# Optimization experiments

Measured on AMD Instinct MI355X. Metric: run time of the kernel, lower is better.

The kernel has to match this reference:

```python
import jax, jax.numpy as jnp
import numpy as np

D = 2048      # d_model
QH = 32       # query heads
KVH = 8       # kv heads
HD = D // QH  # head_dim = 64
B = 2
S = 2048
THETA = 1000000.0


def _rope_cos_sin(seq_len, hd, dtype):
    inv_freq = 1.0 / (THETA ** (jnp.arange(0, hd, 2, dtype=jnp.float32) / hd))
    t = jnp.arange(seq_len, dtype=jnp.float32)
    freqs = jnp.einsum('i,j->ij', t, inv_freq)          # [S, hd/2]
    emb = jnp.concatenate([freqs, freqs], axis=-1)      # [S, hd]
    cos = jnp.cos(emb)[None, :, None, :].astype(dtype)  # [1,S,1,hd]
    sin = jnp.sin(emb)[None, :, None, :].astype(dtype)
    return cos, sin


def _rotate_half(x):
    half = x.shape[-1] // 2
    x1, x2 = x[..., :half], x[..., half:]
    return jnp.concatenate([-x2, x1], axis=-1)


def setup_inputs() -> dict:
    key = jax.random.key(0)
    ks = jax.random.split(key, 9)
    inp = {
        'q': jax.random.normal(ks[0], (B, S, D), dtype=jnp.float32),
        'k': jax.random.normal(ks[1], (B, S, D), dtype=jnp.float32),
        'v': jax.random.normal(ks[2], (B, S, D), dtype=jnp.float32),
        'attn_mask': jnp.ones((B, S), dtype=jnp.float32),  # ignored by source math
        'Wq': jax.random.normal(ks[3], (D, D), dtype=jnp.float32) * 0.02,
        'Wk': jax.random.normal(ks[4], (D, KVH * HD), dtype=jnp.float32) * 0.02,
        'Wv': jax.random.normal(ks[5], (D, KVH * HD), dtype=jnp.float32) * 0.02,
        'Wo': jax.random.normal(ks[6], (D, D), dtype=jnp.float32) * 0.02,
        'bo': jnp.zeros((D,), dtype=jnp.float32),
    }
    return inp


def reference(q, k, v, attn_mask, Wq, Wk, Wv, Wo, bo):
    b, s, _ = q.shape
    qh = (q @ Wq).reshape(b, s, QH, HD)
    kh = (k @ Wk).reshape(b, s, KVH, HD)
    vh = (v @ Wv).reshape(b, s, KVH, HD)

    cos, sin = _rope_cos_sin(s, HD, qh.dtype)
    qh = qh * cos + _rotate_half(qh) * sin
    kh = kh * cos + _rotate_half(kh) * sin

    g = QH // KVH
    # torch .repeat tiles the head axis: [h0..h7, h0..h7, ...]
    kh = jnp.tile(kh, (1, 1, g, 1))  # [b,s,QH,HD]
    vh = jnp.tile(vh, (1, 1, g, 1))

    qt = qh.transpose(0, 2, 1, 3)  # [b,QH,s,HD]
    kt = kh.transpose(0, 2, 1, 3)
    vt = vh.transpose(0, 2, 1, 3)

    scale = 1.0 / jnp.sqrt(jnp.asarray(HD, dtype=qt.dtype))
    scores = jnp.einsum('bhqd,bhkd->bhqk', qt, kt) * scale
    # source passes attn_mask=None, is_causal=False when a mask is given:
    # full non-causal attention, mask value unused.
    attn = jax.nn.softmax(scores, axis=-1)
    out = jnp.einsum('bhqk,bhkd->bhqd', attn, vt)
    out = out.transpose(0, 2, 1, 3).reshape(b, s, D)
    return out @ Wo + bo
```

## Files before the change

### kernel.cpp

```cpp
#include <hip/hip_runtime.h>
#include <math.h>

#define D_    2048
#define QH_   32
#define KVH_  8
#define HD_   64
#define B_    2
#define S_    2048
#define NROW_ (B_*S_)
#define KVD_  (KVH_*HD_)
#define LOG2E 1.44269504f

typedef __bf16 bf16;
typedef __bf16 bf16x2 __attribute__((ext_vector_type(2)));
typedef __bf16 bf16x4 __attribute__((ext_vector_type(4)));
typedef __bf16 bf16x8 __attribute__((ext_vector_type(8)));
typedef float  f32x4  __attribute__((ext_vector_type(4)));
typedef float  f32x16 __attribute__((ext_vector_type(16)));

__device__ __forceinline__ f32x4 mfma16(bf16x8 a, bf16x8 b, f32x4 c) {
  return __builtin_amdgcn_mfma_f32_16x16x32_bf16(a, b, c, 0, 0, 0);
}
__device__ __forceinline__ f32x16 mfma32(bf16x8 a, bf16x8 b, f32x16 c) {
  return __builtin_amdgcn_mfma_f32_32x32x16_bf16(a, b, c, 0, 0, 0);
}

__device__ __forceinline__ void gload_lds16(const bf16* g, bf16* l) {
  __builtin_amdgcn_global_load_lds(
      (const __attribute__((address_space(1))) void*)g,
      (__attribute__((address_space(3))) void*)l, 16, 0, 0);
}

__device__ __forceinline__ unsigned pack_bf16(float a, float b) {
  union { bf16x2 v; unsigned u; } t;
  t.v[0] = (bf16)a; t.v[1] = (bf16)b;
  return t.u;
}

__global__ void k_convert(const float* __restrict__ in, bf16* __restrict__ out, int n4) {
  int i = blockIdx.x * 256 + threadIdx.x;
  if (i >= n4) return;
  f32x4 v = ((const f32x4*)in)[i];
  bf16x4 o;
#pragma unroll
  for (int j = 0; j < 4; j++) o[j] = (bf16)v[j];
  ((bf16x4*)out)[i] = o;
}

__global__ void k_convert2(const float* __restrict__ in0, const float* __restrict__ in1,
                           bf16* __restrict__ o0, bf16* __restrict__ o1, int n4) {
  const float* in = blockIdx.z ? in1 : in0;
  bf16* out = blockIdx.z ? o1 : o0;
  int i = blockIdx.x * 256 + threadIdx.x;
  if (i >= n4) return;
  f32x4 v = ((const f32x4*)in)[i];
  bf16x4 o;
#pragma unroll
  for (int j = 0; j < 4; j++) o[j] = (bf16)v[j];
  ((bf16x4*)out)[i] = o;
}

__device__ __forceinline__ void transpose_w_body(const float* W, bf16* Wt, int K, int N) {
  __shared__ float tile[32][33];
  int n0 = blockIdx.x * 32, k0 = blockIdx.y * 32;
  int tx = threadIdx.x, ty = threadIdx.y;
#pragma unroll
  for (int j = 0; j < 4; j++)
    tile[ty + 8*j][tx] = W[(size_t)(k0 + ty + 8*j) * N + n0 + tx];
  __syncthreads();
#pragma unroll
  for (int j = 0; j < 4; j++)
    Wt[(size_t)(n0 + ty + 8*j) * K + k0 + tx] = (bf16)tile[tx][ty + 8*j];
}

__global__ void k_transpose_w(const float* __restrict__ W, bf16* __restrict__ Wt,
                              int K, int N) {
  transpose_w_body(W, Wt, K, N);
}

__global__ void k_transpose_w2(const float* __restrict__ W0, const float* __restrict__ W1,
                               bf16* __restrict__ T0, bf16* __restrict__ T1) {
  transpose_w_body(blockIdx.z ? W1 : W0, blockIdx.z ? T1 : T0, D_, KVD_);
}

__global__ void k_transpose_v(const bf16* __restrict__ Vh, bf16* __restrict__ Vt) {
  __shared__ float tile[32][33];
  int z = blockIdx.z;
  int b = z >> 3, kv = z & 7;
  int s0 = blockIdx.x * 32, d0 = blockIdx.y * 32;
  int tx = threadIdx.x, ty = threadIdx.y;
#pragma unroll
  for (int j = 0; j < 4; j++)
    tile[ty + 8*j][tx] = (float)Vh[(size_t)(b*S_ + s0 + ty + 8*j) * KVD_ + kv*HD_ + d0 + tx];
  __syncthreads();
#pragma unroll
  for (int j = 0; j < 4; j++)
    Vt[((size_t)z * HD_ + d0 + ty + 8*j) * S_ + s0 + tx] = (bf16)tile[tx][ty + 8*j];
}

__global__ void k_rope(bf16* __restrict__ Qh, bf16* __restrict__ Kh) {
  int t = blockIdx.x * 256 + threadIdx.x;
  int d  = t & 31;
  int hh = (t >> 5) % 40;
  int row = t / 1280;
  if (row >= NROW_) return;
  int s = row & (S_ - 1);
  bf16* p;
  if (hh < QH_) p = Qh + (size_t)row * D_   + hh * HD_;
  else          p = Kh + (size_t)row * KVD_ + (hh - QH_) * HD_;
  float invf = exp2f(-(float)d * 0.62286151f);
  float ang = (float)s * invf;
  float sn, cs;
  sincosf(ang, &sn, &cs);
  float x1 = (float)p[d], x2 = (float)p[d + 32];
  p[d]      = (bf16)(x1 * cs - x2 * sn);
  p[d + 32] = (bf16)(x2 * cs + x1 * sn);
}

template<int OUT_F32_BIAS>
__device__ __forceinline__ void gemm_body(const bf16* A, const bf16* Bt, void* Cout,
                                          const float* bias, int M, int N, int K) {
  __shared__ alignas(16) bf16 As[128 * 32];
  __shared__ alignas(16) bf16 Bs[128 * 32];
  int tid = threadIdx.x;
  int wave = tid >> 6, lane = tid & 63, hi = lane >> 4, lr = lane & 15;
  int wm = wave >> 1, wn = wave & 1;
  int m0 = blockIdx.y * 128, n0 = blockIdx.x * 128;
  f32x4 acc[4][4] = {};
  int nk = K >> 5;
  for (int kt = 0; kt < nk; kt++) {
    int k0 = kt * 32;
#pragma unroll
    for (int i = 0; i < 2; i++) {
      int c = i * 256 + tid;
      int row = c >> 2, slot = c & 3;
      int dch = slot ^ (row & 3);
      gload_lds16(A  + (size_t)(m0 + row) * K + k0 + dch * 8,
                  As + (i * 256 + wave * 64) * 8);
      gload_lds16(Bt + (size_t)(n0 + row) * K + k0 + dch * 8,
                  Bs + (i * 256 + wave * 64) * 8);
    }
    __syncthreads();
    bf16x8 af[4], bfr[4];
#pragma unroll
    for (int mt = 0; mt < 4; mt++) {
      int row = wm * 64 + mt * 16 + lr;
      int slot = hi ^ (row & 3);
      af[mt] = *(const bf16x8*)(As + row * 32 + slot * 8);
    }
#pragma unroll
    for (int nt = 0; nt < 4; nt++) {
      int row = wn * 64 + nt * 16 + lr;
      int slot = hi ^ (row & 3);
      bfr[nt] = *(const bf16x8*)(Bs + row * 32 + slot * 8);
    }
    __builtin_amdgcn_s_setprio(1);
#pragma unroll
    for (int mt = 0; mt < 4; mt++)
#pragma unroll
      for (int nt = 0; nt < 4; nt++)
        acc[mt][nt] = mfma16(af[mt], bfr[nt], acc[mt][nt]);
    __builtin_amdgcn_s_setprio(0);
    __syncthreads();
  }
#pragma unroll
  for (int mt = 0; mt < 4; mt++)
#pragma unroll
    for (int nt = 0; nt < 4; nt++)
#pragma unroll
      for (int r = 0; r < 4; r++) {
        int grow = m0 + wm * 64 + mt * 16 + 4 * hi + r;
        int gcol = n0 + wn * 64 + nt * 16 + lr;
        float v = acc[mt][nt][r];
        if (OUT_F32_BIAS) ((float*)Cout)[(size_t)grow * N + gcol] = v + bias[gcol];
        else              ((bf16*)Cout)[(size_t)grow * N + gcol] = (bf16)v;
      }
}

template<int OUT_F32_BIAS>
__global__ __launch_bounds__(256) void k_gemm(const bf16* __restrict__ A,
                                              const bf16* __restrict__ Bt,
                                              void* __restrict__ Cout,
                                              const float* __restrict__ bias,
                                              int M, int N, int K) {
  gemm_body<OUT_F32_BIAS>(A, Bt, Cout, bias, M, N, K);
}

__global__ __launch_bounds__(256) void k_gemm_kv(const bf16* __restrict__ A0,
                                                 const bf16* __restrict__ A1,
                                                 const bf16* __restrict__ B0,
                                                 const bf16* __restrict__ B1,
                                                 bf16* __restrict__ C0,
                                                 bf16* __restrict__ C1) {
  gemm_body<0>(blockIdx.z ? A1 : A0, blockIdx.z ? B1 : B0,
               blockIdx.z ? (void*)C1 : (void*)C0, nullptr, NROW_, KVD_, D_);
}

__global__ __launch_bounds__(512, 4) void k_attn(const bf16* __restrict__ Qh,
                                                 const bf16* __restrict__ Kh,
                                                 const bf16* __restrict__ Vt,
                                                 bf16* __restrict__ ctx) {
  __shared__ alignas(16) bf16 Ks[2][64 * 64];
  __shared__ alignas(16) bf16 Vs[2][64 * 64];
  int tid = threadIdx.x;
  int wave = tid >> 6, lane = tid & 63, hi2 = lane >> 5, l31 = lane & 31;
  int qt = blockIdx.x, h = blockIdx.y, b = blockIdx.z;
  int kv = h & 7;
  int q0 = qt * 256 + wave * 32;

  bf16x8 qf[4];
  {
    const float QSC = 0.125f * LOG2E;
    const bf16* qp = Qh + (size_t)(b * S_ + q0 + l31) * D_ + h * HD_ + hi2 * 8;
#pragma unroll
    for (int df = 0; df < 4; df++) {
      bf16x8 v = *(const bf16x8*)(qp + 16 * df);
#pragma unroll
      for (int j = 0; j < 8; j++) v[j] = (bf16)((float)v[j] * QSC);
      qf[df] = v;
    }
  }

  f32x16 o0, o1, accl;
#pragma unroll
  for (int i = 0; i < 16; i++) { o0[i] = 0.f; o1[i] = 0.f; accl[i] = 0.f; }
  bf16x8 ones;
#pragma unroll
  for (int j = 0; j < 8; j++) ones[j] = (bf16)1.0f;

  const bf16* Kg = Kh + (size_t)(b * S_) * KVD_ + kv * HD_;
  const bf16* Vg = Vt + (size_t)(b * KVH_ + kv) * HD_ * S_;

  int c_row = tid >> 3, c_slot = tid & 7;
  int c_dch = c_slot ^ (c_row & 7);

#define STAGE(buf, kt_)                                                        \
  do {                                                                         \
    gload_lds16(Kg + (size_t)((kt_) * 64 + c_row) * KVD_ + c_dch * 8,          \
                &Ks[buf][tid * 8]);                                            \
    gload_lds16(Vg + (size_t)c_row * S_ + (kt_) * 64 + c_dch * 8,              \
                &Vs[buf][tid * 8]);                                            \
  } while (0)

  STAGE(0, 0);
  __syncthreads();

  const int NT = S_ / 64;
  for (int kt = 0; kt < NT; kt++) {
    int cur = kt & 1;
    if (kt + 1 < NT) STAGE(cur ^ 1, kt + 1);

    const bf16* Kb = &Ks[cur][0];
    const bf16* Vb = &Vs[cur][0];

    f32x16 s0, s1;
#pragma unroll
    for (int i = 0; i < 16; i++) { s0[i] = 0.f; s1[i] = 0.f; }
    __builtin_amdgcn_s_setprio(1);
#pragma unroll
    for (int df = 0; df < 4; df++) {
      int ch = hi2 + 2 * df;
      int sl = (ch ^ (l31 & 7)) << 3;
      bf16x8 k0 = *(const bf16x8*)(Kb + l31 * 64 + sl);
      bf16x8 k1 = *(const bf16x8*)(Kb + (l31 + 32) * 64 + sl);
      s0 = mfma32(k0, qf[df], s0);
      s1 = mfma32(k1, qf[df], s1);
    }
    __builtin_amdgcn_s_setprio(0);

#pragma unroll
    for (int i = 0; i < 16; i++) s0[i] = __builtin_amdgcn_exp2f(s0[i]);
#pragma unroll
    for (int i = 0; i < 16; i++) s1[i] = __builtin_amdgcn_exp2f(s1[i]);

    unsigned Rk[2][4][2];
#pragma unroll
    for (int m = 0; m < 4; m++)
#pragma unroll
      for (int w = 0; w < 2; w++) {
        Rk[0][m][w] = pack_bf16(s0[4*m + 2*w], s0[4*m + 2*w + 1]);
        Rk[1][m][w] = pack_bf16(s1[4*m + 2*w], s1[4*m + 2*w + 1]);
      }
#pragma unroll
    for (int kf = 0; kf < 2; kf++)
#pragma unroll
      for (int kp = 0; kp < 2; kp++)
#pragma unroll
        for (int w = 0; w < 2; w++)
          asm volatile("v_permlane32_swap_b32 %0, %1"
                       : "+v"(Rk[kf][2*kp][w]), "+v"(Rk[kf][2*kp+1][w]));
    bf16x8 pf[4];
#pragma unroll
    for (int kfr = 0; kfr < 4; kfr++) {
      int kf = kfr >> 1, k2 = (kfr & 1) * 2;
      union { unsigned d[4]; bf16x8 v; } u;
      u.d[0] = Rk[kf][k2][0];     u.d[1] = Rk[kf][k2][1];
      u.d[2] = Rk[kf][k2 + 1][0]; u.d[3] = Rk[kf][k2 + 1][1];
      pf[kfr] = u.v;
    }

    __builtin_amdgcn_s_setprio(1);
#pragma unroll
    for (int kfr = 0; kfr < 4; kfr++) {
      int ch = hi2 + 2 * kfr;
      int sl = (ch ^ (l31 & 7)) << 3;
      bf16x8 v0 = *(const bf16x8*)(Vb + l31 * 64 + sl);
      bf16x8 v1 = *(const bf16x8*)(Vb + (l31 + 32) * 64 + sl);
      o0 = mfma32(pf[kfr], v0, o0);
      o1 = mfma32(pf[kfr], v1, o1);
      accl = mfma32(pf[kfr], ones, accl);
    }
    __builtin_amdgcn_s_setprio(0);
    __syncthreads();
  }
#undef STAGE

#pragma unroll
  for (int r = 0; r < 16; r++) {
    int rowq = (r & 3) + 8 * (r >> 2) + 4 * hi2;
    float inv = 1.f / accl[r];
    size_t base = (size_t)(b * S_ + q0 + rowq) * D_ + h * HD_;
    ctx[base + l31]      = (bf16)(o0[r] * inv);
    ctx[base + l31 + 32] = (bf16)(o1[r] * inv);
  }
}

extern "C" void kernel_launch(void* const* d_in, const int* in_sizes, int n_in,
                              void* d_out, int out_size, void* d_ws, size_t ws_size,
                              hipStream_t stream) {
  const float* q  = (const float*)d_in[0];
  const float* k  = (const float*)d_in[1];
  const float* v  = (const float*)d_in[2];
  const float* Wq = (const float*)d_in[4];
  const float* Wk = (const float*)d_in[5];
  const float* Wv = (const float*)d_in[6];
  const float* Wo = (const float*)d_in[7];
  const float* bo = (const float*)d_in[8];

  char* ws = (char*)d_ws;
  bf16* A0  = (bf16*)(ws + 0);
  bf16* A1  = (bf16*)(ws + 16777216);
  bf16* Wt  = (bf16*)(ws + 33554432);
  bf16* Qh  = (bf16*)(ws + 41943040);
  bf16* Kh  = (bf16*)(ws + 58720256);
  bf16* Vh  = (bf16*)(ws + 62914560);
  bf16* WtK = Wt;
  bf16* WtV = (bf16*)(ws + 33554432 + 2097152);
  bf16* Vtr = A0;
  bf16* ctx = A1;

  const int n4 = NROW_ * D_ / 4;

  k_convert<<<n4 / 256, 256, 0, stream>>>(q, A0, n4);
  k_transpose_w<<<dim3(D_/32, D_/32), dim3(32, 8), 0, stream>>>(Wq, Wt, D_, D_);
  k_gemm<0><<<dim3(D_/128, NROW_/128), 256, 0, stream>>>(A0, Wt, Qh, nullptr, NROW_, D_, D_);
  k_convert2<<<dim3(n4 / 256, 1, 2), 256, 0, stream>>>(k, v, A0, A1, n4);
  k_transpose_w2<<<dim3(KVD_/32, D_/32, 2), dim3(32, 8), 0, stream>>>(Wk, Wv, WtK, WtV);
  k_gemm_kv<<<dim3(KVD_/128, NROW_/128, 2), 256, 0, stream>>>(A0, A1, WtK, WtV, Kh, Vh);
  k_rope<<<(NROW_ * 40 * 32) / 256, 256, 0, stream>>>(Qh, Kh);
  k_transpose_v<<<dim3(S_/32, HD_/32, B_*KVH_), dim3(32, 8), 0, stream>>>(Vh, Vtr);
  k_attn<<<dim3(S_/256, QH_, B_), 512, 0, stream>>>(Qh, Kh, Vtr, ctx);
  k_transpose_w<<<dim3(D_/32, D_/32), dim3(32, 8), 0, stream>>>(Wo, Wt, D_, D_);
  k_gemm<1><<<dim3(D_/128, NROW_/128), 256, 0, stream>>>(ctx, Wt, (float*)d_out, bo, NROW_, D_, D_);
}
```

Baseline: 288.3 us.

## Fuse RoPE into Q/K GEMM epilogues and write V transposed from GEMM

Removes the standalone RoPE kernel and the V transpose kernel. RoPE is applied in the Q and K projection GEMM epilogues using a precomputed cos/sin table; this works because each wave's 64-column tile covers one full head, so dims d and d+32 sit in the same thread. For V, the MFMA operands are swapped so the accumulator comes out transposed and is written straight into the [b, kv*hd, s] layout. This saves two launches and the extra read/write passes over Qh, Kh and Vh, at the cost of an added table kernel and more scattered epilogue stores.

```diff
diff --git a/kernel.cpp b/kernel.cpp
--- a/kernel.cpp
+++ b/kernel.cpp
@@ -37,6 +37,16 @@
   return t.u;
 }
 
+__global__ void k_ropetab(float2* __restrict__ tab) {
+  int idx = blockIdx.x * 256 + threadIdx.x;
+  int s = idx >> 5, d = idx & 31;
+  float invf = exp2f(-(float)d * 0.62286151f);
+  float ang = (float)s * invf;
+  float sn, cs;
+  sincosf(ang, &sn, &cs);
+  tab[idx] = make_float2(cs, sn);
+}
+
 __global__ void k_convert(const float* __restrict__ in, bf16* __restrict__ out, int n4) {
   int i = blockIdx.x * 256 + threadIdx.x;
   if (i >= n4) return;
@@ -83,43 +93,10 @@
   transpose_w_body(blockIdx.z ? W1 : W0, blockIdx.z ? T1 : T0, D_, KVD_);
 }
 
-__global__ void k_transpose_v(const bf16* __restrict__ Vh, bf16* __restrict__ Vt) {
-  __shared__ float tile[32][33];
-  int z = blockIdx.z;
-  int b = z >> 3, kv = z & 7;
-  int s0 = blockIdx.x * 32, d0 = blockIdx.y * 32;
-  int tx = threadIdx.x, ty = threadIdx.y;
-#pragma unroll
-  for (int j = 0; j < 4; j++)
-    tile[ty + 8*j][tx] = (float)Vh[(size_t)(b*S_ + s0 + ty + 8*j) * KVD_ + kv*HD_ + d0 + tx];
-  __syncthreads();
-#pragma unroll
-  for (int j = 0; j < 4; j++)
-    Vt[((size_t)z * HD_ + d0 + ty + 8*j) * S_ + s0 + tx] = (bf16)tile[tx][ty + 8*j];
-}
-
-__global__ void k_rope(bf16* __restrict__ Qh, bf16* __restrict__ Kh) {
-  int t = blockIdx.x * 256 + threadIdx.x;
-  int d  = t & 31;
-  int hh = (t >> 5) % 40;
-  int row = t / 1280;
-  if (row >= NROW_) return;
-  int s = row & (S_ - 1);
-  bf16* p;
-  if (hh < QH_) p = Qh + (size_t)row * D_   + hh * HD_;
-  else          p = Kh + (size_t)row * KVD_ + (hh - QH_) * HD_;
-  float invf = exp2f(-(float)d * 0.62286151f);
-  float ang = (float)s * invf;
-  float sn, cs;
-  sincosf(ang, &sn, &cs);
-  float x1 = (float)p[d], x2 = (float)p[d + 32];
-  p[d]      = (bf16)(x1 * cs - x2 * sn);
-  p[d + 32] = (bf16)(x2 * cs + x1 * sn);
-}
-
-template<int OUT_F32_BIAS>
+template<int EPI>
 __device__ __forceinline__ void gemm_body(const bf16* A, const bf16* Bt, void* Cout,
-                                          const float* bias, int M, int N, int K) {
+                                          const float* bias, const float2* tab,
+                                          int M, int N, int K) {
   __shared__ alignas(16) bf16 As[128 * 32];
   __shared__ alignas(16) bf16 Bs[128 * 32];
   int tid = threadIdx.x;
@@ -158,42 +135,80 @@
 #pragma unroll
     for (int mt = 0; mt < 4; mt++)
 #pragma unroll
-      for (int nt = 0; nt < 4; nt++)
-        acc[mt][nt] = mfma16(af[mt], bfr[nt], acc[mt][nt]);
+      for (int nt = 0; nt < 4; nt++) {
+        if (EPI == 3) acc[mt][nt] = mfma16(bfr[nt], af[mt], acc[mt][nt]);
+        else          acc[mt][nt] = mfma16(af[mt], bfr[nt], acc[mt][nt]);
+      }
     __builtin_amdgcn_s_setprio(0);
     __syncthreads();
   }
-#pragma unroll
-  for (int mt = 0; mt < 4; mt++)
-#pragma unroll
-    for (int nt = 0; nt < 4; nt++)
+
+  if (EPI == 3) {
+    int b = m0 >> 11;
+#pragma unroll
+    for (int mt = 0; mt < 4; mt++)
+#pragma unroll
+      for (int nt = 0; nt < 4; nt++)
+#pragma unroll
+        for (int r = 0; r < 4; r++) {
+          int n = n0 + wn * 64 + nt * 16 + 4 * hi + r;
+          int m = m0 + wm * 64 + mt * 16 + lr;
+          ((bf16*)Cout)[((size_t)(b * KVD_ + n)) * S_ + (m & (S_ - 1))] =
+              (bf16)acc[mt][nt][r];
+        }
+  } else if (EPI == 1) {
+#pragma unroll
+    for (int mt = 0; mt < 4; mt++)
 #pragma unroll
       for (int r = 0; r < 4; r++) {
         int grow = m0 + wm * 64 + mt * 16 + 4 * hi + r;
-        int gcol = n0 + wn * 64 + nt * 16 + lr;
-        float v = acc[mt][nt][r];
-        if (OUT_F32_BIAS) ((float*)Cout)[(size_t)grow * N + gcol] = v + bias[gcol];
-        else              ((bf16*)Cout)[(size_t)grow * N + gcol] = (bf16)v;
+        int s = grow & (S_ - 1);
+#pragma unroll
+        for (int nt = 0; nt < 2; nt++) {
+          int gcol = n0 + wn * 64 + nt * 16 + lr;
+          float2 cs = tab[s * 32 + nt * 16 + lr];
+          float x1 = acc[mt][nt][r], x2 = acc[mt][nt + 2][r];
+          ((bf16*)Cout)[(size_t)grow * N + gcol]      = (bf16)(x1 * cs.x - x2 * cs.y);
+          ((bf16*)Cout)[(size_t)grow * N + gcol + 32] = (bf16)(x2 * cs.x + x1 * cs.y);
+        }
       }
-}
-
-template<int OUT_F32_BIAS>
-__global__ __launch_bounds__(256) void k_gemm(const bf16* __restrict__ A,
-                                              const bf16* __restrict__ Bt,
-                                              void* __restrict__ Cout,
-                                              const float* __restrict__ bias,
-                                              int M, int N, int K) {
-  gemm_body<OUT_F32_BIAS>(A, Bt, Cout, bias, M, N, K);
+  } else {
+#pragma unroll
+    for (int mt = 0; mt < 4; mt++)
+#pragma unroll
+      for (int nt = 0; nt < 4; nt++)
+#pragma unroll
+        for (int r = 0; r < 4; r++) {
+          int grow = m0 + wm * 64 + mt * 16 + 4 * hi + r;
+          int gcol = n0 + wn * 64 + nt * 16 + lr;
+          ((float*)Cout)[(size_t)grow * N + gcol] = acc[mt][nt][r] + bias[gcol];
+        }
+  }
+}
+
+__global__ __launch_bounds__(256) void k_gemm_q(const bf16* __restrict__ A,
+                                                const bf16* __restrict__ Bt,
+                                                bf16* __restrict__ C,
+                                                const float2* __restrict__ tab) {
+  gemm_body<1>(A, Bt, C, nullptr, tab, NROW_, D_, D_);
 }
 
 __global__ __launch_bounds__(256) void k_gemm_kv(const bf16* __restrict__ A0,
                                                  const bf16* __restrict__ A1,
                                                  const bf16* __restrict__ B0,
                                                  const bf16* __restrict__ B1,
-                                                 bf16* __restrict__ C0,
-                                                 bf16* __restrict__ C1) {
-  gemm_body<0>(blockIdx.z ? A1 : A0, blockIdx.z ? B1 : B0,
-               blockIdx.z ? (void*)C1 : (void*)C0, nullptr, NROW_, KVD_, D_);
+                                                 bf16* __restrict__ Kh,
+                                                 bf16* __restrict__ Vt,
+                                                 const float2* __restrict__ tab) {
+  if (blockIdx.z == 0) gemm_body<1>(A0, B0, Kh, nullptr, tab, NROW_, KVD_, D_);
+  else                 gemm_body<3>(A1, B1, Vt, nullptr, nullptr, NROW_, KVD_, D_);
+}
+
+__global__ __launch_bounds__(256) void k_gemm_o(const bf16* __restrict__ A,
+                                                const bf16* __restrict__ Bt,
+                                                float* __restrict__ C,
+                                                const float* __restrict__ bias) {
+  gemm_body<2>(A, Bt, C, bias, nullptr, NROW_, D_, D_);
 }
 
 __global__ __launch_bounds__(512, 4) void k_attn(const bf16* __restrict__ Qh,
@@ -338,28 +353,27 @@
   const float* bo = (const float*)d_in[8];
 
   char* ws = (char*)d_ws;
-  bf16* A0  = (bf16*)(ws + 0);
-  bf16* A1  = (bf16*)(ws + 16777216);
-  bf16* Wt  = (bf16*)(ws + 33554432);
-  bf16* Qh  = (bf16*)(ws + 41943040);
-  bf16* Kh  = (bf16*)(ws + 58720256);
-  bf16* Vh  = (bf16*)(ws + 62914560);
-  bf16* WtK = Wt;
-  bf16* WtV = (bf16*)(ws + 33554432 + 2097152);
-  bf16* Vtr = A0;
-  bf16* ctx = A1;
+  bf16*   A0  = (bf16*)(ws + 0);
+  bf16*   A1  = (bf16*)(ws + 16777216);
+  bf16*   Wt  = (bf16*)(ws + 33554432);
+  bf16*   Qh  = (bf16*)(ws + 41943040);
+  bf16*   Kh  = (bf16*)(ws + 58720256);
+  bf16*   Vt  = (bf16*)(ws + 62914560);
+  float2* tab = (float2*)(ws + 67108864);
+  bf16*   WtK = Wt;
+  bf16*   WtV = (bf16*)(ws + 33554432 + 2097152);
+  bf16*   ctx = A1;
 
   const int n4 = NROW_ * D_ / 4;
 
+  k_ropetab<<<(S_ * 32) / 256, 256, 0, stream>>>(tab);
   k_convert<<<n4 / 256, 256, 0, stream>>>(q, A0, n4);
   k_transpose_w<<<dim3(D_/32, D_/32), dim3(32, 8), 0, stream>>>(Wq, Wt, D_, D_);
-  k_gemm<0><<<dim3(D_/128, NROW_/128), 256, 0, stream>>>(A0, Wt, Qh, nullptr, NROW_, D_, D_);
+  k_gemm_q<<<dim3(D_/128, NROW_/128), 256, 0, stream>>>(A0, Wt, Qh, tab);
   k_convert2<<<dim3(n4 / 256, 1, 2), 256, 0, stream>>>(k, v, A0, A1, n4);
   k_transpose_w2<<<dim3(KVD_/32, D_/32, 2), dim3(32, 8), 0, stream>>>(Wk, Wv, WtK, WtV);
-  k_gemm_kv<<<dim3(KVD_/128, NROW_/128, 2), 256, 0, stream>>>(A0, A1, WtK, WtV, Kh, Vh);
-  k_rope<<<(NROW_ * 40 * 32) / 256, 256, 0, stream>>>(Qh, Kh);
-  k_transpose_v<<<dim3(S_/32, HD_/32, B_*KVH_), dim3(32, 8), 0, stream>>>(Vh, Vtr);
-  k_attn<<<dim3(S_/256, QH_, B_), 512, 0, stream>>>(Qh, Kh, Vtr, ctx);
+  k_gemm_kv<<<dim3(KVD_/128, NROW_/128, 2), 256, 0, stream>>>(A0, A1, WtK, WtV, Kh, Vt, tab);
+  k_attn<<<dim3(S_/256, QH_, B_), 512, 0, stream>>>(Qh, Kh, Vt, ctx);
   k_transpose_w<<<dim3(D_/32, D_/32), dim3(32, 8), 0, stream>>>(Wo, Wt, D_, D_);
-  k_gemm<1><<<dim3(D_/128, NROW_/128), 256, 0, stream>>>(ctx, Wt, (float*)d_out, bo, NROW_, D_, D_);
-}
+  k_gemm_o<<<dim3(D_/128, NROW_/128), 256, 0, stream>>>(ctx, Wt, (float*)d_out, bo);
+}
```

New measurement: 296.7 us. +2.9%, slower.
